# Kernel optimization log

Measured on AMD Instinct MI355X. Metric: run time of the kernel, lower is better.

Reference implementation:

```python
import jax, jax.numpy as jnp
import numpy as np

N = 50000
E = 800000
T = 5            # towers
F = 10           # in_num / F_in per tower (divide_input=False)
F_OUT = 2        # out_channels // towers
G = 64           # number of graphs in the batch
L = 2            # conv layers
BN_EPS = 1e-5
STD_EPS = 1e-5


def setup_inputs() -> dict:
    key = jax.random.key(0)
    ks = jax.random.split(key, 24)
    s = 0.1
    inp = {
        'x': jax.random.normal(ks[0], (N, F), jnp.float32),
        'edge_emb': jax.random.normal(ks[1], (4, F), jnp.float32) * s,
        'mlp1_w1': jax.random.normal(ks[2], (F, 5), jnp.float32) * s,
        'mlp1_b1': jnp.zeros((5,), jnp.float32),
        'mlp1_w2': jax.random.normal(ks[3], (5, F), jnp.float32) * s,
        'mlp1_b2': jnp.zeros((F,), jnp.float32),
        'enc_w': jax.random.normal(ks[4], (L, F, F), jnp.float32) * s,
        'enc_b': jnp.zeros((L, F), jnp.float32),
        'pre_w': jax.random.normal(ks[5], (L, T, 3 * F, F), jnp.float32) * s,
        'pre_b': jnp.zeros((L, T, F), jnp.float32),
        'post_w': jax.random.normal(ks[6], (L, T, 13 * F, F_OUT), jnp.float32) * s,
        'post_b': jnp.zeros((L, T, F_OUT), jnp.float32),
        'lin_w': jax.random.normal(ks[7], (L, F, F), jnp.float32) * s,
        'lin_b': jnp.zeros((L, F), jnp.float32),
        'bn_gamma': jnp.ones((L, F), jnp.float32),
        'bn_beta': jnp.zeros((L, F), jnp.float32),
        'mlp2_w1': jax.random.normal(ks[8], (F, 5), jnp.float32) * s,
        'mlp2_b1': jnp.zeros((5,), jnp.float32),
        'mlp2_w2': jax.random.normal(ks[9], (5, 1), jnp.float32) * s,
        'mlp2_b2': jnp.zeros((1,), jnp.float32),
        'edge_index': jax.random.randint(ks[10], (2, E), 0, N, jnp.int64),
        'edge_attr': jax.random.randint(ks[11], (E,), 0, 4, jnp.int64),
        'batch': jnp.sort(jax.random.randint(ks[12], (N,), 0, G, jnp.int64)),
    }
    return inp


def reference(x, edge_emb, mlp1_w1, mlp1_b1, mlp1_w2, mlp1_b2,
              enc_w, enc_b, pre_w, pre_b, post_w, post_b, lin_w, lin_b,
              bn_gamma, bn_beta, mlp2_w1, mlp2_b1, mlp2_w2, mlp2_b2,
              edge_index, edge_attr, batch):
    src, dst = edge_index[0], edge_index[1]
    # mlp1: 10 -> 5 -> 10
    h = jax.nn.relu(x @ mlp1_w1 + mlp1_b1) @ mlp1_w2 + mlp1_b2  # [N, F]
    ea = edge_emb[edge_attr]  # [E, F] edge embedding lookup

    # in-degree at target nodes, PNA degree statistics
    deg = jax.ops.segment_sum(jnp.ones((src.shape[0],), h.dtype), dst, num_segments=N)
    d = jnp.clip(deg, 1.0)
    avg_log = jnp.mean(jnp.log(deg + 1.0))  # avg_deg['log'] from degree distribution
    log_d = jnp.log(d + 1.0)
    amp = (log_d / avg_log)[:, None, None]
    att = (avg_log / log_d)[:, None, None]
    has_in = (deg > 0)[:, None, None]
    inv_d = (1.0 / d)[:, None, None]

    for l in range(L):
        e = ea @ enc_w[l] + enc_b[l]  # [E, F]
        # message = pre_nn(cat(x_i, x_j, edge_attr)) per tower (x shared across towers)
        msg_in = jnp.concatenate([h[dst], h[src], e], axis=-1)  # [E, 3F]
        m = jnp.einsum('ef,tfo->eto', msg_in, pre_w[l]) + pre_b[l]  # [E, T, F]
        mean = jax.ops.segment_sum(m, dst, num_segments=N) * inv_d
        mean2 = jax.ops.segment_sum(m * m, dst, num_segments=N) * inv_d
        std = jnp.sqrt(jax.nn.relu(mean2 - mean * mean) + STD_EPS)
        mn = jnp.where(has_in, jax.ops.segment_min(m, dst, num_segments=N), 0.0)
        mx = jnp.where(has_in, jax.ops.segment_max(m, dst, num_segments=N), 0.0)
        agg = jnp.concatenate([mean, mn, mx, std], axis=-1)  # [N, T, 4F]
        agg = jnp.concatenate([agg, agg * amp, agg * att], axis=-1)  # [N, T, 12F]
        xt = jnp.broadcast_to(h[:, None, :], (h.shape[0], T, F))
        o = jnp.concatenate([xt, agg], axis=-1)  # [N, T, 13F]
        o = jnp.einsum('ntf,tfo->nto', o, post_w[l]) + post_b[l]  # [N, T, F_OUT]
        o = o.reshape(o.shape[0], T * F_OUT) @ lin_w[l] + lin_b[l]  # [N, F]
        # train-mode BatchNorm over nodes
        mu = jnp.mean(o, axis=0)
        var = jnp.var(o, axis=0)
        o = (o - mu) / jnp.sqrt(var + BN_EPS) * bn_gamma[l] + bn_beta[l]
        h = jax.nn.relu(o)

    g = jax.ops.segment_sum(h, batch, num_segments=G)  # global_add_pool -> [G, F]
    out = jax.nn.relu(g @ mlp2_w1 + mlp2_b1) @ mlp2_w2 + mlp2_b2  # [G, 1]
    return out
```

## Files before the change

### kernel.cpp

```cpp
#include <hip/hip_runtime.h>
#include <math.h>

#define N_NODES 50000
#define N_EDGES 800000
#define G_GRAPHS 64
#define CONV_BLOCKS 2048
#define BSTRIDE 64

#define WAVE_SYNC() asm volatile("s_waitcnt lgkmcnt(0)" ::: "memory")
#define RFL(v) __builtin_amdgcn_readfirstlane(v)

__global__ void k_mlp1(const float* __restrict__ x,
                       const float* __restrict__ w1, const float* __restrict__ b1,
                       const float* __restrict__ w2, const float* __restrict__ b2,
                       float* __restrict__ h,
                       int* __restrict__ cnt,
                       float* __restrict__ bn_part, float* __restrict__ g,
                       float* __restrict__ avg_log,
                       const float* __restrict__ edge_emb,
                       const float* __restrict__ enc_w, const float* __restrict__ enc_b,
                       const float* __restrict__ pre_w, float* __restrict__ encm) {
  __shared__ float eo[2][4][10];
  int tid = threadIdx.x;
  int n = blockIdx.x * blockDim.x + tid;
  if (n < 1280) bn_part[n] = 0.f;
  if (n < G_GRAPHS * 10) g[n] = 0.f;
  if (n == 0) avg_log[0] = 0.f;
  if (n < N_NODES) {
    cnt[n] = 0;
    float xv[10];
#pragma unroll
    for (int k = 0; k < 10; k++) xv[k] = x[n * 10 + k];
    float hid[5];
#pragma unroll
    for (int j = 0; j < 5; j++) {
      float a = b1[j];
#pragma unroll
      for (int k = 0; k < 10; k++) a += xv[k] * w1[k * 5 + j];
      hid[j] = fmaxf(a, 0.f);
    }
#pragma unroll
    for (int f = 0; f < 10; f++) {
      float a = b2[f];
#pragma unroll
      for (int j = 0; j < 5; j++) a += hid[j] * w2[j * 10 + f];
      h[n * 10 + f] = a;
    }
  }
  if (blockIdx.x == 0) {
    for (int i = tid; i < 80; i += 256) {
      int l = i / 40; int a = (i / 10) % 4; int k = i % 10;
      float s = enc_b[l * 10 + k];
      for (int j = 0; j < 10; j++) s += edge_emb[a * 10 + j] * enc_w[(l * 10 + j) * 10 + k];
      eo[l][a][k] = s;
    }
    __syncthreads();
    for (int i = tid; i < 400; i += 256) {
      int l = i / 200; int a = (i / 50) % 4; int t = (i / 10) % 5; int f = i % 10;
      float s = 0.f;
      for (int k = 0; k < 10; k++) s += eo[l][a][k] * pre_w[((l * 5 + t) * 30 + 20 + k) * 10 + f];
      encm[i] = s;
    }
  }
}

__global__ void k_scatter(const int* __restrict__ src, const int* __restrict__ dst,
                          const int* __restrict__ attr,
                          int* __restrict__ cnt, int* __restrict__ epk) {
  int e0 = (blockIdx.x * blockDim.x + threadIdx.x) * 4;
  if (e0 >= N_EDGES) return;
  int4 s = *(const int4*)&src[e0];
  int4 d = *(const int4*)&dst[e0];
  int4 a = *(const int4*)&attr[e0];
  int k;
  k = atomicAdd(&cnt[d.x], 1); if (k < BSTRIDE) epk[d.x * BSTRIDE + k] = s.x | (a.x << 16);
  k = atomicAdd(&cnt[d.y], 1); if (k < BSTRIDE) epk[d.y * BSTRIDE + k] = s.y | (a.y << 16);
  k = atomicAdd(&cnt[d.z], 1); if (k < BSTRIDE) epk[d.z * BSTRIDE + k] = s.z | (a.z << 16);
  k = atomicAdd(&cnt[d.w], 1); if (k < BSTRIDE) epk[d.w * BSTRIDE + k] = s.w | (a.w << 16);
}

__global__ void k_avg(const int* __restrict__ cnt, float* __restrict__ avg_log) {
  __shared__ float ws[4];
  int tid = threadIdx.x;
  float acc = 0.f;
  for (int n = blockIdx.x * 256 + tid; n < N_NODES; n += gridDim.x * 256)
    acc += __logf((float)cnt[n] + 1.f);
#pragma unroll
  for (int d = 32; d >= 1; d >>= 1) acc += __shfl_down(acc, d, 64);
  if ((tid & 63) == 0) ws[tid >> 6] = acc;
  __syncthreads();
  if (tid == 0) atomicAdd(avg_log, ws[0] + ws[1] + ws[2] + ws[3]);
}

__global__ __launch_bounds__(256) void k_u(const float* __restrict__ h,
                                           const float* __restrict__ pre_w_l,
                                           float* __restrict__ u) {
  __shared__ float sw[500];
  int tid = threadIdx.x;
  for (int j = tid; j < 500; j += 256) {
    int t = j / 100, k = (j / 10) % 10, f = j % 10;
    sw[j] = pre_w_l[(t * 30 + 10 + k) * 10 + f];
  }
  __syncthreads();
  int i = blockIdx.x * 256 + tid;
  if (i >= N_NODES * 50) return;
  int n = i / 50, c = i % 50;
  int tb = (c / 10) * 100 + (c % 10);
  const float* hn = h + n * 10;
  float acc = 0.f;
#pragma unroll
  for (int k = 0; k < 10; k++) acc += hn[k] * sw[tb + k * 10];
  u[i] = acc;
}

__global__ __launch_bounds__(256) void k_conv(
    const float* __restrict__ h,
    const float* __restrict__ u,
    const float* __restrict__ pre_w_l,
    const float* __restrict__ pre_b_l,
    const float* __restrict__ post_w_l,
    const float* __restrict__ post_b_l,
    const float* __restrict__ lin_w_l,
    const float* __restrict__ lin_b_l,
    const float* __restrict__ encm_l,
    const int* __restrict__ cnt,
    const int* __restrict__ epk,
    const float* __restrict__ avg_log_p,
    float* __restrict__ o_buf,
    float* __restrict__ bn_part)
{
  __shared__ float sW[1300];
  __shared__ float sLin[100];
  __shared__ float sLb[10];
  __shared__ float sPb[10];
  __shared__ float sP[4][100];
  __shared__ float sO[4][10];
  __shared__ float bnS[10], bnQ[10];

  int tid = threadIdx.x;
  int wid = tid >> 6, lane = tid & 63;
  for (int i = tid; i < 1300; i += 256) sW[i] = post_w_l[i];
  for (int i = tid; i < 100; i += 256) sLin[i] = lin_w_l[i];
  if (tid < 10) {
    sLb[tid] = lin_b_l[tid];
    sPb[tid] = post_b_l[tid];
    bnS[tid] = 0.f; bnQ[tid] = 0.f;
  }
  __syncthreads();

  int f = lane % 10;
  int t = (lane < 50) ? (lane / 10) : 4;
  int c50 = t * 10 + f;
  float wdst[10];
#pragma unroll
  for (int k = 0; k < 10; k++) wdst[k] = pre_w_l[(t * 30 + k) * 10 + f];
  float em0 = encm_l[c50];
  float em1 = encm_l[50 + c50];
  float em2 = encm_l[100 + c50];
  float em3 = encm_l[150 + c50];
  float preb = pre_b_l[c50];
  float avg_log = avg_log_p[0] * (1.f / N_NODES);

  int gw = blockIdx.x * 4 + wid;
  int GW = gridDim.x * 4;
  int nn = (gw < N_NODES) ? ((N_NODES - 1 - gw) / GW + 1) : 0;

  int dgp = 0;
  if (lane < nn) dgp = cnt[gw + lane * GW];

  float bnSv = 0.f, bnQv = 0.f;

#define PRE(US, AS, IDX) { int sp_ = __builtin_amdgcn_readlane(pk, (IDX) & 63); \
    AS = sp_ >> 16; US = 0.f; \
    if ((IDX) < deg) US = u[(sp_ & 0xFFFF) * 50 + c50]; }
#define PROC(US, AS) { float em_ = (AS & 2) ? ((AS & 1) ? em3 : em2) : ((AS & 1) ? em1 : em0); \
    float m_ = base + em_ + US; \
    sum += m_; sq = fmaf(m_, m_, sq); mnv = fminf(mnv, m_); mxv = fmaxf(mxv, m_); }

  int nxt_pk = 0;
  if (nn > 0) {
    int deg0 = RFL(__builtin_amdgcn_readlane(dgp, 0));
    if (deg0 > BSTRIDE) deg0 = BSTRIDE;
    if (lane < deg0) nxt_pk = epk[gw * BSTRIDE + lane];
  }

  for (int i = 0; i < nn; i++) {
    int n = gw + i * GW;
    int deg = RFL(__builtin_amdgcn_readlane(dgp, i));
    if (deg > BSTRIDE) deg = BSTRIDE;
    int pk = nxt_pk;
    if (i + 1 < nn) {
      int degN = RFL(__builtin_amdgcn_readlane(dgp, i + 1));
      if (degN > BSTRIDE) degN = BSTRIDE;
      int nN = gw + (i + 1) * GW;
      nxt_pk = (lane < degN) ? epk[nN * BSTRIDE + lane] : 0;
    }

    const float* hn = h + n * 10;
    float2 d0 = *(const float2*)hn;
    float2 d1 = *(const float2*)(hn + 2);
    float2 d2 = *(const float2*)(hn + 4);
    float2 d3 = *(const float2*)(hn + 6);
    float2 d4 = *(const float2*)(hn + 8);
    float xf = hn[f];
    float base = preb
      + d0.x * wdst[0] + d0.y * wdst[1] + d1.x * wdst[2] + d1.y * wdst[3]
      + d2.x * wdst[4] + d2.y * wdst[5] + d3.x * wdst[6] + d3.y * wdst[7]
      + d4.x * wdst[8] + d4.y * wdst[9];

    float sum = 0.f, sq = 0.f, mnv = INFINITY, mxv = -INFINITY;
    {
      float u0, u1, u2, u3, u4, u5, u6, u7;
      int a0, a1, a2, a3, a4, a5, a6, a7;
      PRE(u0, a0, 0) PRE(u1, a1, 1) PRE(u2, a2, 2) PRE(u3, a3, 3)
      PRE(u4, a4, 4) PRE(u5, a5, 5) PRE(u6, a6, 6) PRE(u7, a7, 7)
      int full = deg & ~7;
      int jb = 0;
      for (; jb < full; jb += 8) {
        PROC(u0, a0) PRE(u0, a0, jb + 8)
        PROC(u1, a1) PRE(u1, a1, jb + 9)
        PROC(u2, a2) PRE(u2, a2, jb + 10)
        PROC(u3, a3) PRE(u3, a3, jb + 11)
        PROC(u4, a4) PRE(u4, a4, jb + 12)
        PROC(u5, a5) PRE(u5, a5, jb + 13)
        PROC(u6, a6) PRE(u6, a6, jb + 14)
        PROC(u7, a7) PRE(u7, a7, jb + 15)
      }
      if (jb + 0 < deg) PROC(u0, a0)
      if (jb + 1 < deg) PROC(u1, a1)
      if (jb + 2 < deg) PROC(u2, a2)
      if (jb + 3 < deg) PROC(u3, a3)
      if (jb + 4 < deg) PROC(u4, a4)
      if (jb + 5 < deg) PROC(u5, a5)
      if (jb + 6 < deg) PROC(u6, a6)
    }

    float degf = (float)deg;
    float d = fmaxf(degf, 1.f);
    float inv = 1.f / d;
    float mean = sum * inv;
    float var = sq * inv - mean * mean;
    float stdv = sqrtf(fmaxf(var, 0.f) + 1e-5f);
    if (deg == 0) { mnv = 0.f; mxv = 0.f; }
    float log_d = logf(d + 1.f);
    float amp = log_d / avg_log;
    float att = avg_log / log_d;

    float vv[13];
    vv[0] = xf;
    vv[1] = mean;       vv[2] = mnv;        vv[3] = mxv;        vv[4] = stdv;
    vv[5] = mean * amp; vv[6] = mnv * amp;  vv[7] = mxv * amp;  vv[8] = stdv * amp;
    vv[9] = mean * att; vv[10] = mnv * att; vv[11] = mxv * att; vv[12] = stdv * att;
    float p0 = 0.f, p1 = 0.f;
#pragma unroll
    for (int j = 0; j < 13; j++) {
      const float2 w = *(const float2*)&sW[t * 260 + (f + 10 * j) * 2];
      p0 += vv[j] * w.x; p1 += vv[j] * w.y;
    }
    if (lane < 50) *(float2*)&sP[wid][c50 * 2] = make_float2(p0, p1);
    WAVE_SYNC();
    if (lane < 10) {
      int tt = lane >> 1, c = lane & 1;
      float o = sPb[lane];
#pragma unroll
      for (int ff = 0; ff < 10; ff++) o += sP[wid][(tt * 10 + ff) * 2 + c];
      sO[wid][lane] = o;
    }
    WAVE_SYNC();
    if (lane < 10) {
      float r = sLb[lane];
#pragma unroll
      for (int j = 0; j < 10; j++) r += sO[wid][j] * sLin[j * 10 + lane];
      o_buf[n * 10 + lane] = r;
      bnSv += r; bnQv += r * r;
    }
    WAVE_SYNC();
  }
#undef PRE
#undef PROC

  if (lane < 10) {
    atomicAdd(&bnS[lane], bnSv);
    atomicAdd(&bnQ[lane], bnQv);
  }
  __syncthreads();
  if (tid < 20) {
    float v = (tid < 10) ? bnS[tid] : bnQ[tid - 10];
    atomicAdd(&bn_part[(blockIdx.x & 31) * 20 + tid], v);
  }
}

__global__ void k_bnpool(const float* __restrict__ o_buf,
                         const float* __restrict__ bn_part,
                         const float* __restrict__ gamma, const float* __restrict__ beta,
                         float* __restrict__ h,
                         const int* __restrict__ batch, float* __restrict__ g,
                         int do_pool) {
  __shared__ float sS[20];
  __shared__ float sMu[10], sInv[10];
  __shared__ float pool[8][10];
  __shared__ int g0s;
  int tid = threadIdx.x;
  if (tid < 20) {
    float s = 0.f;
    for (int j = 0; j < 32; j++) s += bn_part[j * 20 + tid];
    sS[tid] = s;
  }
  if (tid < 80) pool[tid / 10][tid % 10] = 0.f;
  if (tid == 0) {
    int n0 = blockIdx.x * 256 / 10;
    g0s = batch[(n0 < N_NODES) ? n0 : (N_NODES - 1)];
  }
  __syncthreads();
  if (tid < 10) {
    float mu = sS[tid] * (1.f / N_NODES);
    float var = sS[10 + tid] * (1.f / N_NODES) - mu * mu;
    sMu[tid] = mu;
    sInv[tid] = 1.f / sqrtf(fmaxf(var, 0.f) + 1e-5f);
  }
  __syncthreads();
  int i = blockIdx.x * blockDim.x + tid;
  bool act = i < N_NODES * 10;
  if (act) {
    int n = i / 10, f = i % 10;
    float o = (o_buf[i] - sMu[f]) * sInv[f] * gamma[f] + beta[f];
    float r = fmaxf(o, 0.f);
    h[i] = r;
    if (do_pool) {
      int dg = batch[n] - g0s;
      if (dg < 8) atomicAdd(&pool[dg][f], r);
      else atomicAdd(&g[(g0s + dg) * 10 + f], r);
    }
  }
  if (do_pool) {
    __syncthreads();
    if (tid < 80) {
      float v = pool[tid / 10][tid % 10];
      if (v != 0.f) atomicAdd(&g[(g0s + tid / 10) * 10 + tid % 10], v);
    }
  }
}

__global__ void k_mlp2(const float* __restrict__ g,
                       const float* __restrict__ w1, const float* __restrict__ b1,
                       const float* __restrict__ w2, const float* __restrict__ b2,
                       float* __restrict__ out) {
  int b = threadIdx.x;
  if (b >= G_GRAPHS) return;
  float gv[10];
#pragma unroll
  for (int k = 0; k < 10; k++) gv[k] = g[b * 10 + k];
  float acc = b2[0];
#pragma unroll
  for (int j = 0; j < 5; j++) {
    float a = b1[j];
#pragma unroll
    for (int k = 0; k < 10; k++) a += gv[k] * w1[k * 5 + j];
    acc += fmaxf(a, 0.f) * w2[j];
  }
  out[b] = acc;
}

extern "C" void kernel_launch(void* const* d_in, const int* in_sizes, int n_in,
                              void* d_out, int out_size, void* d_ws, size_t ws_size,
                              hipStream_t stream) {
  const float* x        = (const float*)d_in[0];
  const float* edge_emb = (const float*)d_in[1];
  const float* m1w1 = (const float*)d_in[2];
  const float* m1b1 = (const float*)d_in[3];
  const float* m1w2 = (const float*)d_in[4];
  const float* m1b2 = (const float*)d_in[5];
  const float* enc_w = (const float*)d_in[6];
  const float* enc_b = (const float*)d_in[7];
  const float* pre_w = (const float*)d_in[8];
  const float* pre_b = (const float*)d_in[9];
  const float* post_w = (const float*)d_in[10];
  const float* post_b = (const float*)d_in[11];
  const float* lin_w = (const float*)d_in[12];
  const float* lin_b = (const float*)d_in[13];
  const float* bn_g = (const float*)d_in[14];
  const float* bn_b = (const float*)d_in[15];
  const float* m2w1 = (const float*)d_in[16];
  const float* m2b1 = (const float*)d_in[17];
  const float* m2w2 = (const float*)d_in[18];
  const float* m2b2 = (const float*)d_in[19];
  const int* edge_index = (const int*)d_in[20];
  const int* edge_attr  = (const int*)d_in[21];
  const int* batch      = (const int*)d_in[22];
  const int* src  = edge_index;
  const int* dstp = edge_index + N_EDGES;

  char* ws = (char*)d_ws;
  size_t off = 0;
  auto alloc = [&](size_t bytes) {
    void* p = ws + off;
    off += (bytes + 255) & ~(size_t)255;
    return p;
  };
  float*     h       = (float*)alloc(N_NODES * 10 * sizeof(float));
  float*     o_buf   = (float*)alloc(N_NODES * 10 * sizeof(float));
  float*     u       = (float*)alloc((size_t)(N_NODES * 50 + 64) * sizeof(float));
  int*       cnt     = (int*)alloc(N_NODES * sizeof(int));
  int*       epk     = (int*)alloc((size_t)N_NODES * BSTRIDE * sizeof(int));
  float*     encm    = (float*)alloc(400 * sizeof(float));
  float*     avg_log = (float*)alloc(16);
  float*     bn_part = (float*)alloc(2 * 32 * 20 * sizeof(float));
  float*     g       = (float*)alloc(G_GRAPHS * 10 * sizeof(float));

  k_mlp1<<<(N_NODES + 255) / 256, 256, 0, stream>>>(x, m1w1, m1b1, m1w2, m1b2, h,
                                                    cnt, bn_part, g, avg_log,
                                                    edge_emb, enc_w, enc_b, pre_w, encm);
  k_scatter<<<(N_EDGES / 4 + 255) / 256, 256, 0, stream>>>(src, dstp, edge_attr, cnt, epk);
  k_avg<<<64, 256, 0, stream>>>(cnt, avg_log);

  for (int l = 0; l < 2; l++) {
    k_u<<<(N_NODES * 50 + 255) / 256, 256, 0, stream>>>(h, pre_w + l * 1500, u);
    k_conv<<<CONV_BLOCKS, 256, 0, stream>>>(
        h, u, pre_w + l * 1500, pre_b + l * 50, post_w + l * 1300, post_b + l * 10,
        lin_w + l * 100, lin_b + l * 10, encm + l * 200,
        cnt, epk, avg_log, o_buf, bn_part + l * 640);
    k_bnpool<<<(N_NODES * 10 + 255) / 256, 256, 0, stream>>>(
        o_buf, bn_part + l * 640, bn_g + l * 10, bn_b + l * 10, h, batch, g, l == 1);
  }
  k_mlp2<<<1, 64, 0, stream>>>(g, m2w1, m2b1, m2w2, m2b2, (float*)d_out);
}
```

Measured before the change: 288.0 us.

## Fuse per-node u projection into mlp1 and bnpool kernels, drop k_u

Removes the standalone k_u kernel. The per-node projection u = h·pre_w slice is now computed inside k_mlp1 for layer 0 and inside k_bnpool for layer 1, using values already in registers or shared memory. This saves two kernel launches and one reread of h per layer. k_bnpool is re-tiled to 25 nodes per block (250 active threads) so each block has whole node rows available. k_scatter also goes back to one edge per thread instead of four, which trades vectorized loads for more parallelism in the atomics.

```diff
diff --git a/kernel.cpp b/kernel.cpp
--- a/kernel.cpp
+++ b/kernel.cpp
@@ -19,14 +19,19 @@
                        float* __restrict__ avg_log,
                        const float* __restrict__ edge_emb,
                        const float* __restrict__ enc_w, const float* __restrict__ enc_b,
-                       const float* __restrict__ pre_w, float* __restrict__ encm) {
+                       const float* __restrict__ pre_w, float* __restrict__ encm,
+                       float* __restrict__ u) {
   __shared__ float eo[2][4][10];
+  __shared__ float sw[500];
   int tid = threadIdx.x;
   int n = blockIdx.x * blockDim.x + tid;
   if (n < 1280) bn_part[n] = 0.f;
   if (n < G_GRAPHS * 10) g[n] = 0.f;
   if (n == 0) avg_log[0] = 0.f;
-  if (n < N_NODES) {
+
+  bool act = n < N_NODES;
+  float hr[10];
+  if (act) {
     cnt[n] = 0;
     float xv[10];
 #pragma unroll
@@ -44,8 +49,13 @@
       float a = b2[f];
 #pragma unroll
       for (int j = 0; j < 5; j++) a += hid[j] * w2[j * 10 + f];
+      hr[f] = a;
       h[n * 10 + f] = a;
     }
+  }
+  for (int j = tid; j < 500; j += 256) {
+    int t = j / 100, k = (j / 10) % 10, f = j % 10;
+    sw[j] = pre_w[(t * 30 + 10 + k) * 10 + f];
   }
   if (blockIdx.x == 0) {
     for (int i = tid; i < 80; i += 256) {
@@ -54,7 +64,9 @@
       for (int j = 0; j < 10; j++) s += edge_emb[a * 10 + j] * enc_w[(l * 10 + j) * 10 + k];
       eo[l][a][k] = s;
     }
-    __syncthreads();
+  }
+  __syncthreads();
+  if (blockIdx.x == 0) {
     for (int i = tid; i < 400; i += 256) {
       int l = i / 200; int a = (i / 50) % 4; int t = (i / 10) % 5; int f = i % 10;
       float s = 0.f;
@@ -62,21 +74,33 @@
       encm[i] = s;
     }
   }
+  if (act) {
+    float2* up = (float2*)(u + n * 50);
+#pragma unroll
+    for (int c0 = 0; c0 < 25; c0++) {
+      int ca = 2 * c0, cb = 2 * c0 + 1;
+      int ta = ca / 10, fa = ca % 10, tb = cb / 10, fb = cb % 10;
+      float a = 0.f, b = 0.f;
+#pragma unroll
+      for (int k = 0; k < 10; k++) {
+        a += hr[k] * sw[ta * 100 + fa + k * 10];
+        b += hr[k] * sw[tb * 100 + fb + k * 10];
+      }
+      up[c0] = make_float2(a, b);
+    }
+  }
 }
 
 __global__ void k_scatter(const int* __restrict__ src, const int* __restrict__ dst,
                           const int* __restrict__ attr,
                           int* __restrict__ cnt, int* __restrict__ epk) {
-  int e0 = (blockIdx.x * blockDim.x + threadIdx.x) * 4;
-  if (e0 >= N_EDGES) return;
-  int4 s = *(const int4*)&src[e0];
-  int4 d = *(const int4*)&dst[e0];
-  int4 a = *(const int4*)&attr[e0];
-  int k;
-  k = atomicAdd(&cnt[d.x], 1); if (k < BSTRIDE) epk[d.x * BSTRIDE + k] = s.x | (a.x << 16);
-  k = atomicAdd(&cnt[d.y], 1); if (k < BSTRIDE) epk[d.y * BSTRIDE + k] = s.y | (a.y << 16);
-  k = atomicAdd(&cnt[d.z], 1); if (k < BSTRIDE) epk[d.z * BSTRIDE + k] = s.z | (a.z << 16);
-  k = atomicAdd(&cnt[d.w], 1); if (k < BSTRIDE) epk[d.w * BSTRIDE + k] = s.w | (a.w << 16);
+  int e = blockIdx.x * blockDim.x + threadIdx.x;
+  if (e >= N_EDGES) return;
+  int d = dst[e];
+  int s = src[e];
+  int a = attr[e];
+  int k = atomicAdd(&cnt[d], 1);
+  if (k < BSTRIDE) epk[d * BSTRIDE + k] = s | (a << 16);
 }
 
 __global__ void k_avg(const int* __restrict__ cnt, float* __restrict__ avg_log) {
@@ -90,27 +114,6 @@
   if ((tid & 63) == 0) ws[tid >> 6] = acc;
   __syncthreads();
   if (tid == 0) atomicAdd(avg_log, ws[0] + ws[1] + ws[2] + ws[3]);
-}
-
-__global__ __launch_bounds__(256) void k_u(const float* __restrict__ h,
-                                           const float* __restrict__ pre_w_l,
-                                           float* __restrict__ u) {
-  __shared__ float sw[500];
-  int tid = threadIdx.x;
-  for (int j = tid; j < 500; j += 256) {
-    int t = j / 100, k = (j / 10) % 10, f = j % 10;
-    sw[j] = pre_w_l[(t * 30 + 10 + k) * 10 + f];
-  }
-  __syncthreads();
-  int i = blockIdx.x * 256 + tid;
-  if (i >= N_NODES * 50) return;
-  int n = i / 50, c = i % 50;
-  int tb = (c / 10) * 100 + (c % 10);
-  const float* hn = h + n * 10;
-  float acc = 0.f;
-#pragma unroll
-  for (int k = 0; k < 10; k++) acc += hn[k] * sw[tb + k * 10];
-  u[i] = acc;
 }
 
 __global__ __launch_bounds__(256) void k_conv(
@@ -290,27 +293,35 @@
   }
 }
 
-__global__ void k_bnpool(const float* __restrict__ o_buf,
-                         const float* __restrict__ bn_part,
-                         const float* __restrict__ gamma, const float* __restrict__ beta,
-                         float* __restrict__ h,
-                         const int* __restrict__ batch, float* __restrict__ g,
-                         int do_pool) {
+__global__ __launch_bounds__(256) void k_bnpool(
+    const float* __restrict__ o_buf,
+    const float* __restrict__ bn_part,
+    const float* __restrict__ gamma, const float* __restrict__ beta,
+    float* __restrict__ h,
+    const int* __restrict__ batch, float* __restrict__ g,
+    const float* __restrict__ pre_w_next, float* __restrict__ u,
+    int do_u, int do_pool) {
   __shared__ float sS[20];
   __shared__ float sMu[10], sInv[10];
   __shared__ float pool[8][10];
+  __shared__ float hrow[25][10];
+  __shared__ float sw[500];
   __shared__ int g0s;
   int tid = threadIdx.x;
+  int n0 = blockIdx.x * 25;
+  if (do_u) {
+    for (int j = tid; j < 500; j += 256) {
+      int t = j / 100, k = (j / 10) % 10, f = j % 10;
+      sw[j] = pre_w_next[(t * 30 + 10 + k) * 10 + f];
+    }
+  }
   if (tid < 20) {
     float s = 0.f;
     for (int j = 0; j < 32; j++) s += bn_part[j * 20 + tid];
     sS[tid] = s;
   }
   if (tid < 80) pool[tid / 10][tid % 10] = 0.f;
-  if (tid == 0) {
-    int n0 = blockIdx.x * 256 / 10;
-    g0s = batch[(n0 < N_NODES) ? n0 : (N_NODES - 1)];
-  }
+  if (tid == 0) g0s = batch[n0];
   __syncthreads();
   if (tid < 10) {
     float mu = sS[tid] * (1.f / N_NODES);
@@ -319,17 +330,31 @@
     sInv[tid] = 1.f / sqrtf(fmaxf(var, 0.f) + 1e-5f);
   }
   __syncthreads();
-  int i = blockIdx.x * blockDim.x + tid;
-  bool act = i < N_NODES * 10;
-  if (act) {
-    int n = i / 10, f = i % 10;
+  if (tid < 250) {
+    int dn = tid / 10, f = tid % 10;
+    int n = n0 + dn;
+    int i = n * 10 + f;
     float o = (o_buf[i] - sMu[f]) * sInv[f] * gamma[f] + beta[f];
     float r = fmaxf(o, 0.f);
     h[i] = r;
+    hrow[dn][f] = r;
     if (do_pool) {
       int dg = batch[n] - g0s;
       if (dg < 8) atomicAdd(&pool[dg][f], r);
       else atomicAdd(&g[(g0s + dg) * 10 + f], r);
+    }
+  }
+  __syncthreads();
+  if (do_u && tid < 250) {
+#pragma unroll
+    for (int it = 0; it < 5; it++) {
+      int j = tid + it * 250;
+      int node = j / 50, c = j % 50;
+      int t = c / 10, f2 = c % 10;
+      float acc = 0.f;
+#pragma unroll
+      for (int k = 0; k < 10; k++) acc += hrow[node][k] * sw[t * 100 + f2 + k * 10];
+      u[n0 * 50 + j] = acc;
     }
   }
   if (do_pool) {
@@ -409,18 +434,18 @@
 
   k_mlp1<<<(N_NODES + 255) / 256, 256, 0, stream>>>(x, m1w1, m1b1, m1w2, m1b2, h,
                                                     cnt, bn_part, g, avg_log,
-                                                    edge_emb, enc_w, enc_b, pre_w, encm);
-  k_scatter<<<(N_EDGES / 4 + 255) / 256, 256, 0, stream>>>(src, dstp, edge_attr, cnt, epk);
+                                                    edge_emb, enc_w, enc_b, pre_w, encm, u);
+  k_scatter<<<(N_EDGES + 255) / 256, 256, 0, stream>>>(src, dstp, edge_attr, cnt, epk);
   k_avg<<<64, 256, 0, stream>>>(cnt, avg_log);
 
   for (int l = 0; l < 2; l++) {
-    k_u<<<(N_NODES * 50 + 255) / 256, 256, 0, stream>>>(h, pre_w + l * 1500, u);
     k_conv<<<CONV_BLOCKS, 256, 0, stream>>>(
         h, u, pre_w + l * 1500, pre_b + l * 50, post_w + l * 1300, post_b + l * 10,
         lin_w + l * 100, lin_b + l * 10, encm + l * 200,
         cnt, epk, avg_log, o_buf, bn_part + l * 640);
-    k_bnpool<<<(N_NODES * 10 + 255) / 256, 256, 0, stream>>>(
-        o_buf, bn_part + l * 640, bn_g + l * 10, bn_b + l * 10, h, batch, g, l == 1);
+    k_bnpool<<<N_NODES / 25, 256, 0, stream>>>(
+        o_buf, bn_part + l * 640, bn_g + l * 10, bn_b + l * 10, h, batch, g,
+        pre_w + 1500, u, l == 0, l == 1);
   }
   k_mlp2<<<1, 64, 0, stream>>>(g, m2w1, m2b1, m2w2, m2b2, (float*)d_out);
 }
```

Result: no change. 286.7 us (-0.5%).
